# Performance work log

Measured on AMD Instinct MI355X. Metric: run time of the kernel, lower is better.

Reference implementation:

```python
import jax, jax.numpy as jnp
import numpy as np

NUM_CENTROID = 64
HIDDEN = 768
MAX_SEQ = 128
D = MAX_SEQ * HIDDEN  # 98304 flattened feature dim
NUM_ITERS = 10        # fixed Lloyd iterations (original loops to tol; fixed for jit)


def _cdist(x, c):
    x2 = jnp.sum(x * x, axis=-1, keepdims=True)          # [N,1]
    c2 = jnp.sum(c * c, axis=-1)                          # [K]
    d2 = x2 + c2[None, :] - 2.0 * (x @ c.T)               # [N,K]
    return jnp.sqrt(jnp.maximum(d2, 0.0))


def setup_inputs() -> dict:
    key = jax.random.key(0)
    k1, k2 = jax.random.split(key)
    x = jax.random.normal(k1, (1024, MAX_SEQ, HIDDEN), dtype=jnp.float32)
    # centroid table initialized as Normal(mean=0.07, std=0.39) per the module
    centroid = 0.07 + 0.39 * jax.random.normal(k2, (NUM_CENTROID, D), dtype=jnp.float32)
    return {"x": x, "centroid": centroid}


def reference(x, centroid):
    X = x.reshape(-1, D)                                  # [N, D]
    N = X.shape[0]
    # 'resuming' branch: snap each centroid to its nearest sample
    dis0 = _cdist(X, centroid)                            # [N, K]
    choice_points = jnp.argmin(dis0, axis=0)              # [K]
    state = X[choice_points]                              # [K, D]
    ones = jnp.ones((N,), dtype=X.dtype)

    def step(state, _):
        dis = _cdist(X, state)                            # [N, K]
        choice = jnp.argmin(dis, axis=1)                  # [N]
        sums = jax.ops.segment_sum(X, choice, num_segments=NUM_CENTROID)   # [K, D]
        counts = jax.ops.segment_sum(ones, choice, num_segments=NUM_CENTROID)  # [K]
        nonempty = counts[:, None] > 0
        new_state = jnp.where(nonempty, sums / jnp.maximum(counts[:, None], 1.0), state)
        return new_state, choice

    state, choices = jax.lax.scan(step, state, None, length=NUM_ITERS)
    # returns (new centroids, final cluster assignments) like the module
    return state, choices[-1]
```

## Files before the change

### kernel.cpp

```cpp
#include <hip/hip_runtime.h>
#include <cstddef>
#include <cstdint>


#define N_PTS  1024
#define K_C    64
#define D_DIM  98304
#define ITERS  10
#define SPLITD 64
#define BM     64
#define DC     64
#define LDSP   72
#define NCHK   96
#define CCHK   12

typedef __attribute__((ext_vector_type(8))) short bf16x8;
typedef __attribute__((ext_vector_type(4))) float f32x4;

__device__ __forceinline__ unsigned short f2bf(float x) {
    unsigned u = __float_as_uint(x);
    u = (u + 0x7FFFu + ((u >> 16) & 1u)) >> 16;
    return (unsigned short)u;
}
__device__ __forceinline__ float bf2f(unsigned short b) {
    return __uint_as_float((unsigned)b << 16);
}
__device__ __forceinline__ void cvt2(float x, unsigned short& h, unsigned short& l) {
    h = f2bf(x);
    l = f2bf(x - bf2f(h));
}

__device__ __forceinline__ float block_sum256(float s) {
    #pragma unroll
    for (int o = 32; o; o >>= 1) s += __shfl_down(s, o);
    __shared__ float red[4];
    int lane = threadIdx.x & 63, w = threadIdx.x >> 6;
    if (lane == 0) red[w] = s;
    __syncthreads();
    return red[0] + red[1] + red[2] + red[3];
}

__global__ __launch_bounds__(256) void convert_kernel(const float* __restrict__ A,
                                                      unsigned short* __restrict__ Ph,
                                                      unsigned short* __restrict__ Pl,
                                                      float* __restrict__ sq_part) {
    const int n = blockIdx.x, j = blockIdx.y;
    const size_t base = (size_t)n * D_DIM + (size_t)j * 8192;
    const int t = threadIdx.x;
    float ss = 0.f;
    #pragma unroll
    for (int i = 0; i < 4; ++i) {
        size_t e = base + (size_t)i * 2048 + t * 8;
        float4 a = *reinterpret_cast<const float4*>(A + e);
        float4 b = *reinterpret_cast<const float4*>(A + e + 4);
        ss += a.x*a.x + a.y*a.y + a.z*a.z + a.w*a.w;
        ss += b.x*b.x + b.y*b.y + b.z*b.z + b.w*b.w;
        ushort4 h0, l0, h1, l1;
        cvt2(a.x, h0.x, l0.x); cvt2(a.y, h0.y, l0.y);
        cvt2(a.z, h0.z, l0.z); cvt2(a.w, h0.w, l0.w);
        cvt2(b.x, h1.x, l1.x); cvt2(b.y, h1.y, l1.y);
        cvt2(b.z, h1.z, l1.z); cvt2(b.w, h1.w, l1.w);
        *reinterpret_cast<ushort4*>(Ph + e)     = h0;
        *reinterpret_cast<ushort4*>(Ph + e + 4) = h1;
        *reinterpret_cast<ushort4*>(Pl + e)     = l0;
        *reinterpret_cast<ushort4*>(Pl + e + 4) = l1;
    }
    ss = block_sum256(ss);
    if (t == 0) sq_part[n * CCHK + j] = ss;
}

__global__ __launch_bounds__(256) void reduce_sq_kernel(const float* __restrict__ sq_part,
                                                        float* __restrict__ out, int rows) {
    int n = blockIdx.x * 256 + threadIdx.x;
    if (n >= rows) return;
    float s = 0.f;
    #pragma unroll
    for (int j = 0; j < CCHK; ++j) s += sq_part[n * CCHK + j];
    out[n] = s;
}

__global__ __launch_bounds__(256) void mfma_dot_kernel(const unsigned short* __restrict__ Xh,
                                                       const unsigned short* __restrict__ Xl,
                                                       const unsigned short* __restrict__ Sh,
                                                       const unsigned short* __restrict__ Sl,
                                                       float* __restrict__ partial) {
    __shared__ alignas(16) short Ah[BM][LDSP];
    __shared__ alignas(16) short Al[BM][LDSP];
    __shared__ alignas(16) short Bh[K_C][LDSP];
    __shared__ alignas(16) short Bl[K_C][LDSP];

    const int seg = blockIdx.x, nblk = blockIdx.y;
    const int t = threadIdx.x;
    const int wid = t >> 6, lane = t & 63;

    const int d_begin = seg * (D_DIM / SPLITD);
    const int NCH = (D_DIM / SPLITD) / DC;

    const size_t xrow0 = (size_t)(nblk * BM) * D_DIM;
    const int r0 = t >> 3, c0 = (t & 7) * 8;
    const int r1 = (t + 256) >> 3, c1 = c0;

    ushort4 xh0a, xh0b, xh1a, xh1b, xl0a, xl0b, xl1a, xl1b;
    ushort4 sh0a, sh0b, sh1a, sh1b, sl0a, sl0b, sl1a, sl1b;

    auto load_chunk = [&](int d0) {
        const size_t ax0 = xrow0 + (size_t)r0 * D_DIM + d0 + c0;
        const size_t ax1 = xrow0 + (size_t)r1 * D_DIM + d0 + c1;
        const size_t bs0 = (size_t)r0 * D_DIM + d0 + c0;
        const size_t bs1 = (size_t)r1 * D_DIM + d0 + c1;
        xh0a = *reinterpret_cast<const ushort4*>(Xh + ax0);
        xh0b = *reinterpret_cast<const ushort4*>(Xh + ax0 + 4);
        xh1a = *reinterpret_cast<const ushort4*>(Xh + ax1);
        xh1b = *reinterpret_cast<const ushort4*>(Xh + ax1 + 4);
        xl0a = *reinterpret_cast<const ushort4*>(Xl + ax0);
        xl0b = *reinterpret_cast<const ushort4*>(Xl + ax0 + 4);
        xl1a = *reinterpret_cast<const ushort4*>(Xl + ax1);
        xl1b = *reinterpret_cast<const ushort4*>(Xl + ax1 + 4);
        sh0a = *reinterpret_cast<const ushort4*>(Sh + bs0);
        sh0b = *reinterpret_cast<const ushort4*>(Sh + bs0 + 4);
        sh1a = *reinterpret_cast<const ushort4*>(Sh + bs1);
        sh1b = *reinterpret_cast<const ushort4*>(Sh + bs1 + 4);
        sl0a = *reinterpret_cast<const ushort4*>(Sl + bs0);
        sl0b = *reinterpret_cast<const ushort4*>(Sl + bs0 + 4);
        sl1a = *reinterpret_cast<const ushort4*>(Sl + bs1);
        sl1b = *reinterpret_cast<const ushort4*>(Sl + bs1 + 4);
    };
    auto store_chunk = [&]() {
        *reinterpret_cast<ushort4*>(&Ah[r0][c0])     = xh0a;
        *reinterpret_cast<ushort4*>(&Ah[r0][c0 + 4]) = xh0b;
        *reinterpret_cast<ushort4*>(&Ah[r1][c1])     = xh1a;
        *reinterpret_cast<ushort4*>(&Ah[r1][c1 + 4]) = xh1b;
        *reinterpret_cast<ushort4*>(&Al[r0][c0])     = xl0a;
        *reinterpret_cast<ushort4*>(&Al[r0][c0 + 4]) = xl0b;
        *reinterpret_cast<ushort4*>(&Al[r1][c1])     = xl1a;
        *reinterpret_cast<ushort4*>(&Al[r1][c1 + 4]) = xl1b;
        *reinterpret_cast<ushort4*>(&Bh[r0][c0])     = sh0a;
        *reinterpret_cast<ushort4*>(&Bh[r0][c0 + 4]) = sh0b;
        *reinterpret_cast<ushort4*>(&Bh[r1][c1])     = sh1a;
        *reinterpret_cast<ushort4*>(&Bh[r1][c1 + 4]) = sh1b;
        *reinterpret_cast<ushort4*>(&Bl[r0][c0])     = sl0a;
        *reinterpret_cast<ushort4*>(&Bl[r0][c0 + 4]) = sl0b;
        *reinterpret_cast<ushort4*>(&Bl[r1][c1])     = sl1a;
        *reinterpret_cast<ushort4*>(&Bl[r1][c1 + 4]) = sl1b;
    };

    f32x4 acc[4];
    #pragma unroll
    for (int i = 0; i < 4; ++i) acc[i] = f32x4{0.f, 0.f, 0.f, 0.f};

    load_chunk(d_begin);
    for (int c = 0; c < NCH; ++c) {
        __syncthreads();
        store_chunk();
        __syncthreads();
        if (c + 1 < NCH) load_chunk(d_begin + (c + 1) * DC);

        const int ar = wid * 16 + (lane & 15);
        #pragma unroll
        for (int ks = 0; ks < 2; ++ks) {
            const int ko = ks * 32 + (lane >> 4) * 8;
            bf16x8 ah = *reinterpret_cast<const bf16x8*>(&Ah[ar][ko]);
            bf16x8 al = *reinterpret_cast<const bf16x8*>(&Al[ar][ko]);
            #pragma unroll
            for (int nb = 0; nb < 4; ++nb) {
                const int br = nb * 16 + (lane & 15);
                bf16x8 bh = *reinterpret_cast<const bf16x8*>(&Bh[br][ko]);
                bf16x8 bl = *reinterpret_cast<const bf16x8*>(&Bl[br][ko]);
                acc[nb] = __builtin_amdgcn_mfma_f32_16x16x32_bf16(ah, bh, acc[nb], 0, 0, 0);
                acc[nb] = __builtin_amdgcn_mfma_f32_16x16x32_bf16(ah, bl, acc[nb], 0, 0, 0);
                acc[nb] = __builtin_amdgcn_mfma_f32_16x16x32_bf16(al, bh, acc[nb], 0, 0, 0);
            }
        }
    }

    #pragma unroll
    for (int nb = 0; nb < 4; ++nb)
        #pragma unroll
        for (int r = 0; r < 4; ++r) {
            int row = wid * 16 + (lane >> 4) * 4 + r;
            int col = nb * 16 + (lane & 15);
            int n = nblk * BM + row;
            partial[((size_t)seg * N_PTS + n) * K_C + col] = acc[nb][r];
        }
}

__global__ __launch_bounds__(256) void reduce_dot_kernel(const float* __restrict__ partial,
                                                         float* __restrict__ dot) {
    int i = blockIdx.x * 256 + threadIdx.x;
    float s = 0.f;
    #pragma unroll 8
    for (int p = 0; p < SPLITD; ++p) s += partial[(size_t)p * N_PTS * K_C + i];
    dot[i] = s;
}

__global__ __launch_bounds__(256) void argmin_n_kernel(const float* __restrict__ dot,
                                                       const float* __restrict__ x2,
                                                       int* __restrict__ choice_pts) {
    int k = blockIdx.x;
    float best = 3.4e38f; int bi = N_PTS;
    for (int n = threadIdx.x; n < N_PTS; n += 256) {
        float v = fmaf(-2.f, dot[n * K_C + k], x2[n]);
        if (v < best || (v == best && n < bi)) { best = v; bi = n; }
    }
    #pragma unroll
    for (int off = 32; off; off >>= 1) {
        float v2 = __shfl_down(best, off);
        int   i2 = __shfl_down(bi, off);
        if (v2 < best || (v2 == best && i2 < bi)) { best = v2; bi = i2; }
    }
    __shared__ float bv[4]; __shared__ int bix[4];
    int lane = threadIdx.x & 63, wid = threadIdx.x >> 6;
    if (lane == 0) { bv[wid] = best; bix[wid] = bi; }
    __syncthreads();
    if (threadIdx.x == 0) {
        for (int w = 1; w < 4; ++w)
            if (bv[w] < best || (bv[w] == best && bix[w] < bi)) { best = bv[w]; bi = bix[w]; }
        choice_pts[k] = bi;
    }
}

__global__ __launch_bounds__(256) void gather_kernel(const float* __restrict__ X,
                                                     const int* __restrict__ choice_pts,
                                                     float* __restrict__ state) {
    int k = blockIdx.x;
    int c = choice_pts[k];
    size_t d = (size_t)blockIdx.y * 1024 + threadIdx.x * 4;
    float4 v = *reinterpret_cast<const float4*>(X + (size_t)c * D_DIM + d);
    *reinterpret_cast<float4*>(state + (size_t)k * D_DIM + d) = v;
}

__global__ __launch_bounds__(256) void assign_kernel(const float* __restrict__ partial,
                                                     const float* __restrict__ c2p,
                                                     int* __restrict__ choice) {
    int wid = threadIdx.x >> 6, lane = threadIdx.x & 63;
    int n = blockIdx.x * 4 + wid;
    float s = 0.f;
    #pragma unroll 8
    for (int p = 0; p < SPLITD; ++p) s += partial[((size_t)p * N_PTS + n) * K_C + lane];
    float c2 = 0.f;
    #pragma unroll
    for (int j = 0; j < CCHK; ++j) c2 += c2p[lane * CCHK + j];
    float v = fmaf(-2.f, s, c2);
    int bi = lane;
    #pragma unroll
    for (int m = 32; m; m >>= 1) {
        float v2 = __shfl_xor(v, m);
        int   i2 = __shfl_xor(bi, m);
        if (v2 < v || (v2 == v && i2 < bi)) { v = v2; bi = i2; }
    }
    if (lane == 0) choice[n] = bi;
}

__global__ __launch_bounds__(256) void init_prev_kernel(int* __restrict__ chp,
                                                        int* __restrict__ ctp) {
    int t = blockIdx.x * 256 + threadIdx.x;
    if (t < N_PTS) chp[t] = -1;
    if (t < K_C)   ctp[t] = 0;
}

__global__ __launch_bounds__(1024) void changes_kernel(const int* __restrict__ ch_new,
                                                       const int* __restrict__ ch_prev,
                                                       int* __restrict__ add_n,
                                                       int* __restrict__ astart,
                                                       int* __restrict__ sub_n,
                                                       int* __restrict__ sstart,
                                                       int* __restrict__ counts_new) {
    __shared__ int chn[N_PTS];
    __shared__ int chp[N_PTS];
    __shared__ int acnt[K_C], scnt[K_C], hcnt[K_C];
    __shared__ int ast[K_C + 1], sst[K_C + 1];
    const int t = threadIdx.x;
    if (t < K_C) { acnt[t] = 0; scnt[t] = 0; hcnt[t] = 0; }
    __syncthreads();
    const int cn = ch_new[t], cp = ch_prev[t];
    chn[t] = cn; chp[t] = cp;
    atomicAdd(&hcnt[cn], 1);
    const bool changed = (cn != cp);
    if (changed) {
        atomicAdd(&acnt[cn], 1);
        if (cp >= 0) atomicAdd(&scnt[cp], 1);
    }
    __syncthreads();
    if (t == 0) {
        int a = 0;
        for (int k = 0; k < K_C; ++k) { ast[k] = a; a += acnt[k]; }
        ast[K_C] = a;
    }
    if (t == 1 || blockDim.x == 1) { }
    if (t == 64) {
        int a = 0;
        for (int k = 0; k < K_C; ++k) { sst[k] = a; a += scnt[k]; }
        sst[K_C] = a;
    }
    __syncthreads();
    int ra = 0, rs = 0;
    for (int m = 0; m < t; ++m) {
        int cm = chn[m], pm = chp[m];
        bool ch = (cm != pm);
        ra += (ch && cm == cn);
        rs += (ch && pm == cp);
    }
    if (changed) {
        add_n[ast[cn] + ra] = t;
        if (cp >= 0) sub_n[sst[cp] + rs] = t;
    }
    if (t <= K_C) { astart[t] = ast[t]; sstart[t] = sst[t]; }
    if (t < K_C) counts_new[t] = hcnt[t];
}

__global__ __launch_bounds__(256) void update_kernel(const float* __restrict__ X,
                                                     const int* __restrict__ add_n,
                                                     const int* __restrict__ astart,
                                                     const int* __restrict__ sub_n,
                                                     const int* __restrict__ sstart,
                                                     const int* __restrict__ counts_new,
                                                     const int* __restrict__ counts_prev,
                                                     float* __restrict__ state) {
    const int k = blockIdx.x;
    const int ab = astart[k], ae = astart[k + 1];
    const int sb = sstart[k], se = sstart[k + 1];
    if (ab == ae && sb == se) return;
    const int cn = counts_new[k], cp = counts_prev[k];
    const size_t d = (size_t)blockIdx.y * 1024 + threadIdx.x * 4;
    float* sp = state + (size_t)k * D_DIM + d;

    float sx = 0.f, sy = 0.f, sz = 0.f, sw = 0.f;
    if (cp > 0) {
        float4 st = *reinterpret_cast<const float4*>(sp);
        float c = (float)cp;
        sx = st.x * c; sy = st.y * c; sz = st.z * c; sw = st.w * c;
    }
    for (int i = ab; i < ae; ++i) {
        const float4 v = *reinterpret_cast<const float4*>(X + (size_t)add_n[i] * D_DIM + d);
        sx += v.x; sy += v.y; sz += v.z; sw += v.w;
    }
    for (int i = sb; i < se; ++i) {
        const float4 v = *reinterpret_cast<const float4*>(X + (size_t)sub_n[i] * D_DIM + d);
        sx -= v.x; sy -= v.y; sz -= v.z; sw -= v.w;
    }
    if (cn > 0) {
        float inv = 1.f / (float)cn;
        float4 o; o.x = sx * inv; o.y = sy * inv; o.z = sz * inv; o.w = sw * inv;
        *reinterpret_cast<float4*>(sp) = o;
    }
}

__global__ __launch_bounds__(256) void choice_out_kernel(const int* __restrict__ choice,
                                                         float* __restrict__ out) {
    int n = blockIdx.x * 256 + threadIdx.x;
    if (n < N_PTS) out[n] = (float)choice[n];
}

extern "C" void kernel_launch(void* const* d_in, const int* in_sizes, int n_in,
                              void* d_out, int out_size, void* d_ws, size_t ws_size,
                              hipStream_t stream) {
    const float* X  = (const float*)d_in[0];
    const float* C0 = (const float*)d_in[1];
    float* state      = (float*)d_out;
    float* out_choice = state + (size_t)K_C * D_DIM;

    char* w = (char*)d_ws;
    size_t off = 0;
    auto alloc = [&](size_t bytes) { void* p = w + off; off = (off + bytes + 255) & ~(size_t)255; return p; };
    unsigned short* Xh = (unsigned short*)alloc((size_t)N_PTS * D_DIM * 2);
    unsigned short* Xl = (unsigned short*)alloc((size_t)N_PTS * D_DIM * 2);
    unsigned short* Sh = (unsigned short*)alloc((size_t)K_C * D_DIM * 2);
    unsigned short* Sl = (unsigned short*)alloc((size_t)K_C * D_DIM * 2);
    float* partial = (float*)alloc((size_t)SPLITD * N_PTS * K_C * 4);
    float* dotb    = (float*)alloc((size_t)N_PTS * K_C * 4);
    float* x2p     = (float*)alloc((size_t)N_PTS * CCHK * 4);
    float* x2      = (float*)alloc((size_t)N_PTS * 4);
    float* c2p     = (float*)alloc((size_t)K_C * CCHK * 4);
    int* cpts      = (int*)alloc(256);
    int* ch[2];
    ch[0] = (int*)alloc((size_t)N_PTS * 4);
    ch[1] = (int*)alloc((size_t)N_PTS * 4);
    int* ct[2];
    ct[0] = (int*)alloc(256);
    ct[1] = (int*)alloc(256);
    int* add_n  = (int*)alloc((size_t)N_PTS * 4);
    int* astart = (int*)alloc(512);
    int* sub_n  = (int*)alloc((size_t)N_PTS * 4);
    int* sstart = (int*)alloc(512);

    dim3 b256(256);

    convert_kernel<<<dim3(N_PTS, CCHK), b256, 0, stream>>>(X, Xh, Xl, x2p);
    reduce_sq_kernel<<<dim3(4), b256, 0, stream>>>(x2p, x2, N_PTS);

    convert_kernel<<<dim3(K_C, CCHK), b256, 0, stream>>>(C0, Sh, Sl, c2p);
    mfma_dot_kernel<<<dim3(SPLITD, N_PTS / BM), b256, 0, stream>>>(Xh, Xl, Sh, Sl, partial);
    reduce_dot_kernel<<<dim3(N_PTS * K_C / 256), b256, 0, stream>>>(partial, dotb);
    argmin_n_kernel<<<K_C, b256, 0, stream>>>(dotb, x2, cpts);
    gather_kernel<<<dim3(K_C, NCHK), b256, 0, stream>>>(X, cpts, state);
    init_prev_kernel<<<dim3(4), b256, 0, stream>>>(ch[0], ct[0]);

    for (int it = 0; it < ITERS; ++it) {
        int prev = it & 1, cur = 1 - prev;
        convert_kernel<<<dim3(K_C, CCHK), b256, 0, stream>>>(state, Sh, Sl, c2p);
        mfma_dot_kernel<<<dim3(SPLITD, N_PTS / BM), b256, 0, stream>>>(Xh, Xl, Sh, Sl, partial);
        assign_kernel<<<dim3(N_PTS / 4), b256, 0, stream>>>(partial, c2p, ch[cur]);
        changes_kernel<<<1, dim3(1024), 0, stream>>>(ch[cur], ch[prev], add_n, astart,
                                                     sub_n, sstart, ct[cur]);
        update_kernel<<<dim3(K_C, NCHK), b256, 0, stream>>>(X, add_n, astart, sub_n, sstart,
                                                            ct[cur], ct[prev], state);
    }

    choice_out_kernel<<<dim3(N_PTS / 256), b256, 0, stream>>>(ch[0], out_choice);
}
```

Baseline: 2.004 ms.

## Load A fragments directly from global, fuse centroid conversion into gather/update

The dot kernel now reads X hi/lo fragments straight from global memory into MFMA registers instead of staging them in LDS. Only centroid tiles go through shared memory, and the loop is double-buffered over two chunks with a launch-bounds occupancy hint. The per-iteration convert_kernel on the state is removed: gather and update now write the bf16 hi/lo split and the per-chunk squared norms directly, and assign sums 96 partials per centroid. This cuts LDS traffic and one full pass over the state each iteration. In exchange, global A loads are less coalesced (each row is read as 16-byte fragments) and register pressure rises.

```diff
diff --git a/kernel.cpp b/kernel.cpp
--- a/kernel.cpp
+++ b/kernel.cpp
@@ -15,6 +15,7 @@
 #define CCHK   12
 
 typedef __attribute__((ext_vector_type(8))) short bf16x8;
+typedef __attribute__((ext_vector_type(8))) unsigned short ushort8;
 typedef __attribute__((ext_vector_type(4))) float f32x4;
 
 __device__ __forceinline__ unsigned short f2bf(float x) {
@@ -79,99 +80,100 @@
     out[n] = s;
 }
 
-__global__ __launch_bounds__(256) void mfma_dot_kernel(const unsigned short* __restrict__ Xh,
-                                                       const unsigned short* __restrict__ Xl,
-                                                       const unsigned short* __restrict__ Sh,
-                                                       const unsigned short* __restrict__ Sl,
-                                                       float* __restrict__ partial) {
-    __shared__ alignas(16) short Ah[BM][LDSP];
-    __shared__ alignas(16) short Al[BM][LDSP];
+__global__ __launch_bounds__(256, 5) void mfma_dot_kernel(const unsigned short* __restrict__ Xh,
+                                                          const unsigned short* __restrict__ Xl,
+                                                          const unsigned short* __restrict__ Sh,
+                                                          const unsigned short* __restrict__ Sl,
+                                                          float* __restrict__ partial) {
     __shared__ alignas(16) short Bh[K_C][LDSP];
     __shared__ alignas(16) short Bl[K_C][LDSP];
 
     const int seg = blockIdx.x, nblk = blockIdx.y;
     const int t = threadIdx.x;
     const int wid = t >> 6, lane = t & 63;
-
     const int d_begin = seg * (D_DIM / SPLITD);
     const int NCH = (D_DIM / SPLITD) / DC;
 
-    const size_t xrow0 = (size_t)(nblk * BM) * D_DIM;
-    const int r0 = t >> 3, c0 = (t & 7) * 8;
-    const int r1 = (t + 256) >> 3, c1 = c0;
-
-    ushort4 xh0a, xh0b, xh1a, xh1b, xl0a, xl0b, xl1a, xl1b;
-    ushort4 sh0a, sh0b, sh1a, sh1b, sl0a, sl0b, sl1a, sl1b;
-
-    auto load_chunk = [&](int d0) {
-        const size_t ax0 = xrow0 + (size_t)r0 * D_DIM + d0 + c0;
-        const size_t ax1 = xrow0 + (size_t)r1 * D_DIM + d0 + c1;
-        const size_t bs0 = (size_t)r0 * D_DIM + d0 + c0;
-        const size_t bs1 = (size_t)r1 * D_DIM + d0 + c1;
-        xh0a = *reinterpret_cast<const ushort4*>(Xh + ax0);
-        xh0b = *reinterpret_cast<const ushort4*>(Xh + ax0 + 4);
-        xh1a = *reinterpret_cast<const ushort4*>(Xh + ax1);
-        xh1b = *reinterpret_cast<const ushort4*>(Xh + ax1 + 4);
-        xl0a = *reinterpret_cast<const ushort4*>(Xl + ax0);
-        xl0b = *reinterpret_cast<const ushort4*>(Xl + ax0 + 4);
-        xl1a = *reinterpret_cast<const ushort4*>(Xl + ax1);
-        xl1b = *reinterpret_cast<const ushort4*>(Xl + ax1 + 4);
-        sh0a = *reinterpret_cast<const ushort4*>(Sh + bs0);
-        sh0b = *reinterpret_cast<const ushort4*>(Sh + bs0 + 4);
-        sh1a = *reinterpret_cast<const ushort4*>(Sh + bs1);
-        sh1b = *reinterpret_cast<const ushort4*>(Sh + bs1 + 4);
-        sl0a = *reinterpret_cast<const ushort4*>(Sl + bs0);
-        sl0b = *reinterpret_cast<const ushort4*>(Sl + bs0 + 4);
-        sl1a = *reinterpret_cast<const ushort4*>(Sl + bs1);
-        sl1b = *reinterpret_cast<const ushort4*>(Sl + bs1 + 4);
+    const int arow = nblk * BM + wid * 16 + (lane & 15);
+    const int ko = (lane >> 4) * 8;
+    const unsigned short* xh = Xh + (size_t)arow * D_DIM;
+    const unsigned short* xl = Xl + (size_t)arow * D_DIM;
+
+    const int sr = t >> 2, sc = (t & 3) * 16;
+    const unsigned short* shp = Sh + (size_t)sr * D_DIM;
+    const unsigned short* slp = Sl + (size_t)sr * D_DIM;
+
+    ushort8 s0, s1, s2, s3;
+    bf16x8 aEh0, aEh1, aEl0, aEl1;
+    bf16x8 aOh0, aOh1, aOl0, aOl1;
+
+    auto loadB = [&](int d0) {
+        s0 = *reinterpret_cast<const ushort8*>(shp + d0 + sc);
+        s1 = *reinterpret_cast<const ushort8*>(shp + d0 + sc + 8);
+        s2 = *reinterpret_cast<const ushort8*>(slp + d0 + sc);
+        s3 = *reinterpret_cast<const ushort8*>(slp + d0 + sc + 8);
     };
-    auto store_chunk = [&]() {
-        *reinterpret_cast<ushort4*>(&Ah[r0][c0])     = xh0a;
-        *reinterpret_cast<ushort4*>(&Ah[r0][c0 + 4]) = xh0b;
-        *reinterpret_cast<ushort4*>(&Ah[r1][c1])     = xh1a;
-        *reinterpret_cast<ushort4*>(&Ah[r1][c1 + 4]) = xh1b;
-        *reinterpret_cast<ushort4*>(&Al[r0][c0])     = xl0a;
-        *reinterpret_cast<ushort4*>(&Al[r0][c0 + 4]) = xl0b;
-        *reinterpret_cast<ushort4*>(&Al[r1][c1])     = xl1a;
-        *reinterpret_cast<ushort4*>(&Al[r1][c1 + 4]) = xl1b;
-        *reinterpret_cast<ushort4*>(&Bh[r0][c0])     = sh0a;
-        *reinterpret_cast<ushort4*>(&Bh[r0][c0 + 4]) = sh0b;
-        *reinterpret_cast<ushort4*>(&Bh[r1][c1])     = sh1a;
-        *reinterpret_cast<ushort4*>(&Bh[r1][c1 + 4]) = sh1b;
-        *reinterpret_cast<ushort4*>(&Bl[r0][c0])     = sl0a;
-        *reinterpret_cast<ushort4*>(&Bl[r0][c0 + 4]) = sl0b;
-        *reinterpret_cast<ushort4*>(&Bl[r1][c1])     = sl1a;
-        *reinterpret_cast<ushort4*>(&Bl[r1][c1 + 4]) = sl1b;
+    auto storeB = [&]() {
+        *reinterpret_cast<ushort8*>(&Bh[sr][sc])     = s0;
+        *reinterpret_cast<ushort8*>(&Bh[sr][sc + 8]) = s1;
+        *reinterpret_cast<ushort8*>(&Bl[sr][sc])     = s2;
+        *reinterpret_cast<ushort8*>(&Bl[sr][sc + 8]) = s3;
     };
 
     f32x4 acc[4];
     #pragma unroll
     for (int i = 0; i < 4; ++i) acc[i] = f32x4{0.f, 0.f, 0.f, 0.f};
 
-    load_chunk(d_begin);
-    for (int c = 0; c < NCH; ++c) {
+    #define LOADA(bh0, bh1, bl0, bl1, d0)                                        \
+        bh0 = *reinterpret_cast<const bf16x8*>(xh + (d0) + ko);                  \
+        bh1 = *reinterpret_cast<const bf16x8*>(xh + (d0) + 32 + ko);             \
+        bl0 = *reinterpret_cast<const bf16x8*>(xl + (d0) + ko);                  \
+        bl1 = *reinterpret_cast<const bf16x8*>(xl + (d0) + 32 + ko);
+
+    #define MFMAS(ah0, ah1, al0, al1)                                            \
+        _Pragma("unroll")                                                        \
+        for (int nb = 0; nb < 4; ++nb) {                                         \
+            const int br = nb * 16 + (lane & 15);                                \
+            bf16x8 bh = *reinterpret_cast<const bf16x8*>(&Bh[br][ko]);           \
+            bf16x8 bl = *reinterpret_cast<const bf16x8*>(&Bl[br][ko]);           \
+            acc[nb] = __builtin_amdgcn_mfma_f32_16x16x32_bf16(ah0, bh, acc[nb], 0, 0, 0); \
+            acc[nb] = __builtin_amdgcn_mfma_f32_16x16x32_bf16(ah0, bl, acc[nb], 0, 0, 0); \
+            acc[nb] = __builtin_amdgcn_mfma_f32_16x16x32_bf16(al0, bh, acc[nb], 0, 0, 0); \
+        }                                                                        \
+        _Pragma("unroll")                                                        \
+        for (int nb = 0; nb < 4; ++nb) {                                         \
+            const int br = nb * 16 + (lane & 15);                                \
+            bf16x8 bh = *reinterpret_cast<const bf16x8*>(&Bh[br][32 + ko]);      \
+            bf16x8 bl = *reinterpret_cast<const bf16x8*>(&Bl[br][32 + ko]);      \
+            acc[nb] = __builtin_amdgcn_mfma_f32_16x16x32_bf16(ah1, bh, acc[nb], 0, 0, 0); \
+            acc[nb] = __builtin_amdgcn_mfma_f32_16x16x32_bf16(ah1, bl, acc[nb], 0, 0, 0); \
+            acc[nb] = __builtin_amdgcn_mfma_f32_16x16x32_bf16(al1, bh, acc[nb], 0, 0, 0); \
+        }
+
+    loadB(d_begin);
+    LOADA(aEh0, aEh1, aEl0, aEl1, d_begin);
+    for (int c = 0; c < NCH; c += 2) {
         __syncthreads();
-        store_chunk();
+        storeB();
         __syncthreads();
-        if (c + 1 < NCH) load_chunk(d_begin + (c + 1) * DC);
-
-        const int ar = wid * 16 + (lane & 15);
-        #pragma unroll
-        for (int ks = 0; ks < 2; ++ks) {
-            const int ko = ks * 32 + (lane >> 4) * 8;
-            bf16x8 ah = *reinterpret_cast<const bf16x8*>(&Ah[ar][ko]);
-            bf16x8 al = *reinterpret_cast<const bf16x8*>(&Al[ar][ko]);
-            #pragma unroll
-            for (int nb = 0; nb < 4; ++nb) {
-                const int br = nb * 16 + (lane & 15);
-                bf16x8 bh = *reinterpret_cast<const bf16x8*>(&Bh[br][ko]);
-                bf16x8 bl = *reinterpret_cast<const bf16x8*>(&Bl[br][ko]);
-                acc[nb] = __builtin_amdgcn_mfma_f32_16x16x32_bf16(ah, bh, acc[nb], 0, 0, 0);
-                acc[nb] = __builtin_amdgcn_mfma_f32_16x16x32_bf16(ah, bl, acc[nb], 0, 0, 0);
-                acc[nb] = __builtin_amdgcn_mfma_f32_16x16x32_bf16(al, bh, acc[nb], 0, 0, 0);
-            }
+        {
+            int dn = d_begin + (c + 1) * DC;
+            loadB(dn);
+            LOADA(aOh0, aOh1, aOl0, aOl1, dn);
         }
-    }
+        MFMAS(aEh0, aEh1, aEl0, aEl1);
+        __syncthreads();
+        storeB();
+        __syncthreads();
+        if (c + 2 < NCH) {
+            int dn = d_begin + (c + 2) * DC;
+            loadB(dn);
+            LOADA(aEh0, aEh1, aEl0, aEl1, dn);
+        }
+        MFMAS(aOh0, aOh1, aOl0, aOl1);
+    }
+    #undef LOADA
+    #undef MFMAS
 
     #pragma unroll
     for (int nb = 0; nb < 4; ++nb)
@@ -221,12 +223,22 @@
 
 __global__ __launch_bounds__(256) void gather_kernel(const float* __restrict__ X,
                                                      const int* __restrict__ choice_pts,
-                                                     float* __restrict__ state) {
+                                                     float* __restrict__ state,
+                                                     unsigned short* __restrict__ Sh,
+                                                     unsigned short* __restrict__ Sl,
+                                                     float* __restrict__ c2p) {
     int k = blockIdx.x;
     int c = choice_pts[k];
     size_t d = (size_t)blockIdx.y * 1024 + threadIdx.x * 4;
+    size_t o = (size_t)k * D_DIM + d;
     float4 v = *reinterpret_cast<const float4*>(X + (size_t)c * D_DIM + d);
-    *reinterpret_cast<float4*>(state + (size_t)k * D_DIM + d) = v;
+    *reinterpret_cast<float4*>(state + o) = v;
+    ushort4 h, l;
+    cvt2(v.x, h.x, l.x); cvt2(v.y, h.y, l.y); cvt2(v.z, h.z, l.z); cvt2(v.w, h.w, l.w);
+    *reinterpret_cast<ushort4*>(Sh + o) = h;
+    *reinterpret_cast<ushort4*>(Sl + o) = l;
+    float ss = block_sum256(v.x*v.x + v.y*v.y + v.z*v.z + v.w*v.w);
+    if (threadIdx.x == 0) c2p[k * NCHK + blockIdx.y] = ss;
 }
 
 __global__ __launch_bounds__(256) void assign_kernel(const float* __restrict__ partial,
@@ -238,8 +250,9 @@
     #pragma unroll 8
     for (int p = 0; p < SPLITD; ++p) s += partial[((size_t)p * N_PTS + n) * K_C + lane];
     float c2 = 0.f;
-    #pragma unroll
-    for (int j = 0; j < CCHK; ++j) c2 += c2p[lane * CCHK + j];
+    const float* cp2 = c2p + lane * NCHK;
+    #pragma unroll 8
+    for (int j = 0; j < NCHK; ++j) c2 += cp2[j];
     float v = fmaf(-2.f, s, c2);
     int bi = lane;
     #pragma unroll
@@ -286,7 +299,6 @@
         for (int k = 0; k < K_C; ++k) { ast[k] = a; a += acnt[k]; }
         ast[K_C] = a;
     }
-    if (t == 1 || blockDim.x == 1) { }
     if (t == 64) {
         int a = 0;
         for (int k = 0; k < K_C; ++k) { sst[k] = a; a += scnt[k]; }
@@ -315,18 +327,21 @@
                                                      const int* __restrict__ sstart,
                                                      const int* __restrict__ counts_new,
                                                      const int* __restrict__ counts_prev,
-                                                     float* __restrict__ state) {
+                                                     float* __restrict__ state,
+                                                     unsigned short* __restrict__ Sh,
+                                                     unsigned short* __restrict__ Sl,
+                                                     float* __restrict__ c2p) {
     const int k = blockIdx.x;
     const int ab = astart[k], ae = astart[k + 1];
     const int sb = sstart[k], se = sstart[k + 1];
     if (ab == ae && sb == se) return;
     const int cn = counts_new[k], cp = counts_prev[k];
     const size_t d = (size_t)blockIdx.y * 1024 + threadIdx.x * 4;
-    float* sp = state + (size_t)k * D_DIM + d;
+    const size_t o = (size_t)k * D_DIM + d;
 
     float sx = 0.f, sy = 0.f, sz = 0.f, sw = 0.f;
     if (cp > 0) {
-        float4 st = *reinterpret_cast<const float4*>(sp);
+        float4 st = *reinterpret_cast<const float4*>(state + o);
         float c = (float)cp;
         sx = st.x * c; sy = st.y * c; sz = st.z * c; sw = st.w * c;
     }
@@ -340,8 +355,14 @@
     }
     if (cn > 0) {
         float inv = 1.f / (float)cn;
-        float4 o; o.x = sx * inv; o.y = sy * inv; o.z = sz * inv; o.w = sw * inv;
-        *reinterpret_cast<float4*>(sp) = o;
+        float4 m; m.x = sx * inv; m.y = sy * inv; m.z = sz * inv; m.w = sw * inv;
+        *reinterpret_cast<float4*>(state + o) = m;
+        ushort4 h, l;
+        cvt2(m.x, h.x, l.x); cvt2(m.y, h.y, l.y); cvt2(m.z, h.z, l.z); cvt2(m.w, h.w, l.w);
+        *reinterpret_cast<ushort4*>(Sh + o) = h;
+        *reinterpret_cast<ushort4*>(Sl + o) = l;
+        float ss = block_sum256(m.x*m.x + m.y*m.y + m.z*m.z + m.w*m.w);
+        if (threadIdx.x == 0) c2p[k * NCHK + blockIdx.y] = ss;
     }
 }
 
@@ -370,7 +391,8 @@
     float* dotb    = (float*)alloc((size_t)N_PTS * K_C * 4);
     float* x2p     = (float*)alloc((size_t)N_PTS * CCHK * 4);
     float* x2      = (float*)alloc((size_t)N_PTS * 4);
-    float* c2p     = (float*)alloc((size_t)K_C * CCHK * 4);
+    float* c0sq    = (float*)alloc((size_t)K_C * CCHK * 4);
+    float* c2p     = (float*)alloc((size_t)K_C * NCHK * 4);
     int* cpts      = (int*)alloc(256);
     int* ch[2];
     ch[0] = (int*)alloc((size_t)N_PTS * 4);
@@ -388,22 +410,21 @@
     convert_kernel<<<dim3(N_PTS, CCHK), b256, 0, stream>>>(X, Xh, Xl, x2p);
     reduce_sq_kernel<<<dim3(4), b256, 0, stream>>>(x2p, x2, N_PTS);
 
-    convert_kernel<<<dim3(K_C, CCHK), b256, 0, stream>>>(C0, Sh, Sl, c2p);
+    convert_kernel<<<dim3(K_C, CCHK), b256, 0, stream>>>(C0, Sh, Sl, c0sq);
     mfma_dot_kernel<<<dim3(SPLITD, N_PTS / BM), b256, 0, stream>>>(Xh, Xl, Sh, Sl, partial);
     reduce_dot_kernel<<<dim3(N_PTS * K_C / 256), b256, 0, stream>>>(partial, dotb);
     argmin_n_kernel<<<K_C, b256, 0, stream>>>(dotb, x2, cpts);
-    gather_kernel<<<dim3(K_C, NCHK), b256, 0, stream>>>(X, cpts, state);
+    gather_kernel<<<dim3(K_C, NCHK), b256, 0, stream>>>(X, cpts, state, Sh, Sl, c2p);
     init_prev_kernel<<<dim3(4), b256, 0, stream>>>(ch[0], ct[0]);
 
     for (int it = 0; it < ITERS; ++it) {
         int prev = it & 1, cur = 1 - prev;
-        convert_kernel<<<dim3(K_C, CCHK), b256, 0, stream>>>(state, Sh, Sl, c2p);
         mfma_dot_kernel<<<dim3(SPLITD, N_PTS / BM), b256, 0, stream>>>(Xh, Xl, Sh, Sl, partial);
         assign_kernel<<<dim3(N_PTS / 4), b256, 0, stream>>>(partial, c2p, ch[cur]);
         changes_kernel<<<1, dim3(1024), 0, stream>>>(ch[cur], ch[prev], add_n, astart,
                                                      sub_n, sstart, ct[cur]);
         update_kernel<<<dim3(K_C, NCHK), b256, 0, stream>>>(X, add_n, astart, sub_n, sstart,
-                                                            ct[cur], ct[prev], state);
+                                                            ct[cur], ct[prev], state, Sh, Sl, c2p);
     }
 
     choice_out_kernel<<<dim3(N_PTS / 256), b256, 0, stream>>>(ch[0], out_choice);
```

Result: no change. 2.011 ms (+0.4%).
